# Performance work log

Measured on AMD Instinct MI355X. Metric: run time of the kernel, lower is better.

The kernel has to match this reference:

```python
import jax, jax.numpy as jnp
import numpy as np

B, NPG, D_IN, D, L = 64, 512, 1, 128, 10
N = B * NPG
DEG = 16
E = N * DEG
EPS = 1e-5


def setup_inputs() -> dict:
    key = jax.random.key(0)
    ks = jax.random.split(key, 8)
    x = jax.random.normal(ks[0], (N, D_IN), jnp.float32)
    # edges confined within each graph: local indices + per-graph offset
    src_local = jax.random.randint(ks[1], (E,), 0, NPG)
    dst_local = jax.random.randint(ks[2], (E,), 0, NPG)
    offs = (jnp.arange(E) // (E // B)) * NPG
    edge_src = (src_local + offs).astype(jnp.int32)
    edge_dst = (dst_local + offs).astype(jnp.int32)
    batch = jnp.repeat(jnp.arange(B, dtype=jnp.int32), NPG)
    g = lambda k, s, fan: jax.random.normal(k, s, jnp.float32) / np.float32(np.sqrt(fan))
    W0 = g(ks[3], (D_IN, D), D_IN)
    b0 = jnp.zeros((D,), jnp.float32)
    W_rest = g(ks[4], (L - 1, D, D), D)
    b_rest = jnp.zeros((L - 1, D), jnp.float32)
    gamma = jnp.ones((L, D), jnp.float32)
    beta = jnp.zeros((L, D), jnp.float32)
    W_att = g(ks[5], (D, D), D)
    return dict(x=x, edge_src=edge_src, edge_dst=edge_dst, batch=batch,
                W0=W0, b0=b0, W_rest=W_rest, b_rest=b_rest,
                gamma=gamma, beta=beta, W_att=W_att)


def _gcn_conv(h, W, b, src, dst, norm_e, self_w):
    # GCNConv: h' = D^-1/2 (A + I) D^-1/2 (h W) + b  (symmetric norm, self-loops)
    h = h @ W
    msg = norm_e[:, None] * h[src]                      # [E, D] gather
    agg = jax.ops.segment_sum(msg, dst, num_segments=N)  # [N, D] scatter-add
    return agg + self_w[:, None] * h + b


def _bn_relu(h, g, b):
    mu = jnp.mean(h, axis=0)
    var = jnp.var(h, axis=0)
    return jax.nn.relu(g * (h - mu) * jax.lax.rsqrt(var + EPS) + b)


def reference(x, edge_src, edge_dst, batch, W0, b0, W_rest, b_rest, gamma, beta, W_att):
    # symmetric GCN normalization with self-loops (edge weight 1)
    deg = 1.0 + jax.ops.segment_sum(jnp.ones((E,), x.dtype), edge_dst, num_segments=N)
    dinv = jax.lax.rsqrt(deg)
    norm_e = dinv[edge_src] * dinv[edge_dst]   # [E]
    self_w = dinv * dinv                        # [N] self-loop coefficient

    h = _gcn_conv(x, W0, b0, edge_src, edge_dst, norm_e, self_w)
    h = _bn_relu(h, gamma[0], beta[0])
    for l in range(L - 1):
        h = _gcn_conv(h, W_rest[l], b_rest[l], edge_src, edge_dst, norm_e, self_w)
        h = _bn_relu(h, gamma[l + 1], beta[l + 1])

    # graph attention pooling
    mean = jax.ops.segment_sum(h, batch, num_segments=B) / jnp.float32(NPG)  # [B, D]
    tg = jnp.tanh(mean @ W_att)                                              # [B, D]
    coefs = jax.nn.sigmoid(jnp.sum(h * tg[batch], axis=1) * 10.0)            # [N]
    graph_feat = jax.ops.segment_sum(coefs[:, None] * h, batch, num_segments=B)  # [B, D]

    # to_dense_batch (equal-sized graphs -> exact reshape) + concat broadcast graph feat
    node_dense = h.reshape(B, NPG, D)
    gf = jnp.broadcast_to(graph_feat[:, None, :], (B, NPG, D))
    return jnp.concatenate([node_dense, gf], axis=-1)  # [B, NPG, 2D]
```

## Files before the change

### kernel.cpp

```cpp
#include <hip/hip_runtime.h>
#include <hip/hip_bf16.h>
#include <math.h>

#define NN 32768
#define BG 64
#define NPGC 512
#define DD 128
#define EE 524288
#define LL 10
#define EPSF 1e-5f
#define PADK 72

typedef __attribute__((ext_vector_type(8))) short short8;
typedef __attribute__((ext_vector_type(4))) float float4v;

static __device__ __forceinline__ unsigned short f2bf(float x) {
    __hip_bfloat16 b = __float2bfloat16(x);
    return *reinterpret_cast<unsigned short*>(&b);
}
static __device__ __forceinline__ float bf2f(unsigned short u) {
    unsigned int v = ((unsigned int)u) << 16;
    return __uint_as_float(v);
}
static __device__ __forceinline__ void splitbf(float x, unsigned short& h, unsigned short& l) {
    unsigned short hh = f2bf(x);
    h = hh;
    l = f2bf(x - bf2f(hh));
}


__global__ void k_hist(const int* __restrict__ dst, int* __restrict__ cnt) {
    int e = blockIdx.x * 256 + threadIdx.x;
    atomicAdd(&cnt[dst[e]], 1);
}

__global__ void k_dinv(const int* __restrict__ cnt, float* __restrict__ dinv) {
    int n = blockIdx.x * 256 + threadIdx.x;
    dinv[n] = rsqrtf(1.0f + (float)cnt[n]);
}

__global__ void k_scan(const int* __restrict__ cnt, int* __restrict__ rp) {
    __shared__ int s[1024];
    int t = threadIdx.x;
    int loc[32];
    int base = t * 32, tot = 0;
    for (int i = 0; i < 32; i++) { loc[i] = cnt[base + i]; tot += loc[i]; }
    s[t] = tot;
    __syncthreads();
    for (int off = 1; off < 1024; off <<= 1) {
        int add = (t >= off) ? s[t - off] : 0;
        __syncthreads();
        s[t] += add;
        __syncthreads();
    }
    int ex = (t == 0) ? 0 : s[t - 1];
    for (int i = 0; i < 32; i++) { rp[base + i] = ex; ex += loc[i]; }
    if (t == 1023) rp[NN] = ex;
}

__global__ void k_fill(const int* __restrict__ src, const int* __restrict__ dst,
                       const float* __restrict__ dinv, const int* __restrict__ rp,
                       int* __restrict__ cursor, int* __restrict__ csr_src,
                       float* __restrict__ csr_w) {
    int e = blockIdx.x * 256 + threadIdx.x;
    int d = dst[e], sx = src[e];
    int p = atomicAdd(&cursor[d], 1);
    int i = rp[d] + p;
    csr_src[i] = sx;
    csr_w[i] = dinv[sx] * dinv[d];
}

__global__ __launch_bounds__(256) void k_adj(const int* __restrict__ rp,
        const int* __restrict__ csr_src, const float* __restrict__ csr_w,
        const float* __restrict__ dinv, unsigned short* __restrict__ Adj_h,
        unsigned short* __restrict__ Adj_l) {
    __shared__ float rowbuf[4][512];
    int t = threadIdx.x, lane = t & 63, wv = t >> 6;
    int n = blockIdx.x * 4 + wv;
    int nl = n & 511;
    for (int j = lane; j < 512; j += 64) rowbuf[wv][j] = 0.f;
    __syncthreads();
    int e1 = rp[n + 1];
    for (int e = rp[n] + lane; e < e1; e += 64)
        atomicAdd(&rowbuf[wv][csr_src[e] & 511], csr_w[e]);
    __syncthreads();
    if (lane == 0) rowbuf[wv][nl] += dinv[n] * dinv[n];
    __syncthreads();
    size_t base = (size_t)n * 512;
    for (int j = lane; j < 512; j += 64) {
        unsigned short h, l;
        splitbf(rowbuf[wv][j], h, l);
        Adj_h[base + j] = h;
        Adj_l[base + j] = l;
    }
}

__global__ void k_wt(const float* __restrict__ Wr, unsigned short* __restrict__ Wt_h,
                     unsigned short* __restrict__ Wt_l) {
    int idx = blockIdx.x * 256 + threadIdx.x;
    int l = idx >> 14, rem = idx & 16383;
    int fp = rem >> 7, f = rem & 127;
    unsigned short h, lo;
    splitbf(Wr[l * 16384 + f * 128 + fp], h, lo);
    Wt_h[idx] = h;
    Wt_l[idx] = lo;
}

__global__ void k_l0(const float* __restrict__ x, const float* __restrict__ W0,
                     unsigned short* __restrict__ hwT_h, unsigned short* __restrict__ hwT_l) {
    int u = blockIdx.x * 256 + threadIdx.x;
    int f = u >> 12, n0 = (u & 4095) * 8;
    float w = W0[f];
    float4 xa = *(const float4*)(x + n0);
    float4 xb = *(const float4*)(x + n0 + 4);
    float v[8] = {xa.x * w, xa.y * w, xa.z * w, xa.w * w,
                  xb.x * w, xb.y * w, xb.z * w, xb.w * w};
    unsigned short uh[8], ul[8];
    #pragma unroll
    for (int i = 0; i < 8; i++) splitbf(v[i], uh[i], ul[i]);
    *(uint4*)(hwT_h + (size_t)f * NN + n0) = *(uint4*)uh;
    *(uint4*)(hwT_l + (size_t)f * NN + n0) = *(uint4*)ul;
}

__global__ __launch_bounds__(256) void k_aggmm(const unsigned short* __restrict__ Adj_h,
        const unsigned short* __restrict__ Adj_l, const unsigned short* __restrict__ hwT_h,
        const unsigned short* __restrict__ hwT_l, const float* __restrict__ bias,
        float* __restrict__ pre, float* __restrict__ stats) {
    __shared__ unsigned short As_h[64 * PADK], As_l[64 * PADK];
    __shared__ unsigned short Bs_h[128 * PADK], Bs_l[128 * PADK];
    __shared__ float s_bias[128];
    __shared__ float s_sum[128], s_sq[128];
    int t = threadIdx.x, lane = t & 63, wv = t >> 6;
    int l15 = lane & 15, quad = lane >> 4;
    int b = blockIdx.x, r = b & 7, q = b >> 3;
    int g = r + 8 * (q & 7);
    int mb = (q >> 3) * 64;
    size_t arow = ((size_t)g * 512 + mb) * 512;
    size_t gcol = (size_t)g * 512;
    if (t < 128) { s_bias[t] = bias[t]; s_sum[t] = 0.f; s_sq[t] = 0.f; }
    float4v acc[8];
    #pragma unroll
    for (int i = 0; i < 8; i++) acc[i] = (float4v)0.f;

    for (int kc = 0; kc < 512; kc += 64) {
        __syncthreads();
        #pragma unroll
        for (int i = 0; i < 2; i++) {
            int u = t + i * 256;
            int row = u >> 3, ko = (u & 7) * 8;
            size_t go = arow + (size_t)row * 512 + kc + ko;
            *(uint4*)(&As_h[row * PADK + ko]) = *(const uint4*)(Adj_h + go);
            *(uint4*)(&As_l[row * PADK + ko]) = *(const uint4*)(Adj_l + go);
        }
        #pragma unroll
        for (int i = 0; i < 4; i++) {
            int u = t + i * 256;
            int f = u >> 3, ko = (u & 7) * 8;
            size_t go = (size_t)f * NN + gcol + kc + ko;
            *(uint4*)(&Bs_h[f * PADK + ko]) = *(const uint4*)(hwT_h + go);
            *(uint4*)(&Bs_l[f * PADK + ko]) = *(const uint4*)(hwT_l + go);
        }
        __syncthreads();
        int m0 = wv * 16;
        #pragma unroll
        for (int ks = 0; ks < 2; ks++) {
            int kb = ks * 32 + quad * 8;
            short8 ah = *(const short8*)(&As_h[(m0 + l15) * PADK + kb]);
            short8 al = *(const short8*)(&As_l[(m0 + l15) * PADK + kb]);
            #pragma unroll
            for (int nt = 0; nt < 8; nt++) {
                short8 bh = *(const short8*)(&Bs_h[(nt * 16 + l15) * PADK + kb]);
                short8 bl = *(const short8*)(&Bs_l[(nt * 16 + l15) * PADK + kb]);
                acc[nt] = __builtin_amdgcn_mfma_f32_16x16x32_bf16(ah, bh, acc[nt], 0, 0, 0);
                acc[nt] = __builtin_amdgcn_mfma_f32_16x16x32_bf16(ah, bl, acc[nt], 0, 0, 0);
                acc[nt] = __builtin_amdgcn_mfma_f32_16x16x32_bf16(al, bh, acc[nt], 0, 0, 0);
            }
        }
    }
    int n0 = g * 512 + mb + wv * 16 + quad * 4;
    #pragma unroll
    for (int nt = 0; nt < 8; nt++) {
        int f = nt * 16 + l15;
        float bf = s_bias[f];
        float cs = 0.f, cq = 0.f;
        #pragma unroll
        for (int rg = 0; rg < 4; rg++) {
            float v = acc[nt][rg] + bf;
            pre[(size_t)(n0 + rg) * 128 + f] = v;
            cs += v;
            cq = fmaf(v, v, cq);
        }
        cs += __shfl_xor(cs, 16); cs += __shfl_xor(cs, 32);
        cq += __shfl_xor(cq, 16); cq += __shfl_xor(cq, 32);
        if (quad == 0) { atomicAdd(&s_sum[f], cs); atomicAdd(&s_sq[f], cq); }
    }
    __syncthreads();
    if (t < 128) {
        atomicAdd(&stats[t], s_sum[t]);
        atomicAdd(&stats[128 + t], s_sq[t]);
    }
}

__global__ __launch_bounds__(256) void k_mmT(const float* __restrict__ pre,
        const float* __restrict__ stats, const float* __restrict__ gamma,
        const float* __restrict__ beta, const unsigned short* __restrict__ Wt_h,
        const unsigned short* __restrict__ Wt_l, unsigned short* __restrict__ hwT_h,
        unsigned short* __restrict__ hwT_l) {
    __shared__ unsigned short Ws_h[128 * PADK], Ws_l[128 * PADK];
    __shared__ unsigned short Xs_h[64 * PADK], Xs_l[64 * PADK];
    __shared__ float scL[256];
    int t = threadIdx.x, lane = t & 63, wv = t >> 6;
    int l15 = lane & 15, quad = lane >> 4;
    int b = blockIdx.x, r = b & 7, q = b >> 3;
    int g = r + 8 * (q & 7);
    int nb = g * NPGC + (q >> 3) * 64;
    if (t < 128) {
        float mu = stats[t] * (1.0f / NN);
        float var = stats[128 + t] * (1.0f / NN) - mu * mu;
        float s = gamma[t] * rsqrtf(var + EPSF);
        scL[t] = s;
        scL[128 + t] = fmaf(-mu, s, beta[t]);
    }
    float4v acc[8];
    #pragma unroll
    for (int i = 0; i < 8; i++) acc[i] = (float4v)0.f;

    for (int kc = 0; kc < 128; kc += 64) {
        __syncthreads();
        #pragma unroll
        for (int i = 0; i < 4; i++) {
            int u = t + i * 256;
            int fp = u >> 3, ko = (u & 7) * 8;
            int go = fp * 128 + kc + ko;
            *(uint4*)(&Ws_h[fp * PADK + ko]) = *(const uint4*)(Wt_h + go);
            *(uint4*)(&Ws_l[fp * PADK + ko]) = *(const uint4*)(Wt_l + go);
        }
        #pragma unroll
        for (int i = 0; i < 2; i++) {
            int u = t + i * 256;
            int n = u >> 3, fo = (u & 7) * 8;
            const float* pp = pre + (size_t)(nb + n) * 128 + kc + fo;
            float4 v0 = *(const float4*)(pp);
            float4 v1 = *(const float4*)(pp + 4);
            float4 s0 = *(const float4*)(&scL[kc + fo]);
            float4 s1 = *(const float4*)(&scL[kc + fo + 4]);
            float4 h0 = *(const float4*)(&scL[128 + kc + fo]);
            float4 h1 = *(const float4*)(&scL[128 + kc + fo + 4]);
            float v[8] = {fmaxf(fmaf(v0.x, s0.x, h0.x), 0.f),
                          fmaxf(fmaf(v0.y, s0.y, h0.y), 0.f),
                          fmaxf(fmaf(v0.z, s0.z, h0.z), 0.f),
                          fmaxf(fmaf(v0.w, s0.w, h0.w), 0.f),
                          fmaxf(fmaf(v1.x, s1.x, h1.x), 0.f),
                          fmaxf(fmaf(v1.y, s1.y, h1.y), 0.f),
                          fmaxf(fmaf(v1.z, s1.z, h1.z), 0.f),
                          fmaxf(fmaf(v1.w, s1.w, h1.w), 0.f)};
            unsigned short uh[8], ul[8];
            #pragma unroll
            for (int j = 0; j < 8; j++) splitbf(v[j], uh[j], ul[j]);
            *(uint4*)(&Xs_h[n * PADK + fo]) = *(uint4*)uh;
            *(uint4*)(&Xs_l[n * PADK + fo]) = *(uint4*)ul;
        }
        __syncthreads();
        int m0 = wv * 32;
        #pragma unroll
        for (int ks = 0; ks < 2; ks++) {
            int kb = ks * 32 + quad * 8;
            short8 a0h = *(const short8*)(&Ws_h[(m0 + l15) * PADK + kb]);
            short8 a0l = *(const short8*)(&Ws_l[(m0 + l15) * PADK + kb]);
            short8 a1h = *(const short8*)(&Ws_h[(m0 + 16 + l15) * PADK + kb]);
            short8 a1l = *(const short8*)(&Ws_l[(m0 + 16 + l15) * PADK + kb]);
            #pragma unroll
            for (int nt = 0; nt < 4; nt++) {
                short8 bh = *(const short8*)(&Xs_h[(nt * 16 + l15) * PADK + kb]);
                short8 bl = *(const short8*)(&Xs_l[(nt * 16 + l15) * PADK + kb]);
                acc[nt]     = __builtin_amdgcn_mfma_f32_16x16x32_bf16(a0h, bh, acc[nt], 0, 0, 0);
                acc[nt]     = __builtin_amdgcn_mfma_f32_16x16x32_bf16(a0h, bl, acc[nt], 0, 0, 0);
                acc[nt]     = __builtin_amdgcn_mfma_f32_16x16x32_bf16(a0l, bh, acc[nt], 0, 0, 0);
                acc[4 + nt] = __builtin_amdgcn_mfma_f32_16x16x32_bf16(a1h, bh, acc[4 + nt], 0, 0, 0);
                acc[4 + nt] = __builtin_amdgcn_mfma_f32_16x16x32_bf16(a1h, bl, acc[4 + nt], 0, 0, 0);
                acc[4 + nt] = __builtin_amdgcn_mfma_f32_16x16x32_bf16(a1l, bh, acc[4 + nt], 0, 0, 0);
            }
        }
    }
    #pragma unroll
    for (int mt = 0; mt < 2; mt++) {
        #pragma unroll
        for (int nt = 0; nt < 4; nt++) {
            int n = nb + nt * 16 + l15;
            int fp0 = wv * 32 + mt * 16 + quad * 4;
            float4v a = acc[mt * 4 + nt];
            #pragma unroll
            for (int rg = 0; rg < 4; rg++) {
                unsigned short h, lo;
                splitbf(a[rg], h, lo);
                hwT_h[(size_t)(fp0 + rg) * NN + n] = h;
                hwT_l[(size_t)(fp0 + rg) * NN + n] = lo;
            }
        }
    }
}

__global__ __launch_bounds__(256) void k_bn_pool(float* __restrict__ pre,
        const float* __restrict__ stats, const float* __restrict__ gamma,
        const float* __restrict__ beta, float* __restrict__ meansum) {
    __shared__ float ssum[256];
    __shared__ float scL[256];
    int t = threadIdx.x;
    int b = blockIdx.x, r = b & 7, q = b >> 3;
    int g = r + 8 * (q & 7);
    int nb = g * NPGC + (q >> 3) * 64;
    if (t < 128) {
        float mu = stats[t] * (1.0f / NN);
        float var = stats[128 + t] * (1.0f / NN) - mu * mu;
        float s = gamma[t] * rsqrtf(var + EPSF);
        scL[t] = s;
        scL[128 + t] = fmaf(-mu, s, beta[t]);
    }
    __syncthreads();
    int f = t & 127;
    float s = scL[f], sh = scL[128 + f];
    float lsum = 0.f;
    int base = nb * 128;
    for (int i = 0; i < 32; i++) {
        int idx = base + i * 256 + t;
        float v = fmaxf(fmaf(pre[idx], s, sh), 0.f);
        pre[idx] = v;
        lsum += v;
    }
    ssum[t] = lsum;
    __syncthreads();
    if (t < 128) atomicAdd(&meansum[g * 128 + f], ssum[t] + ssum[t + 128]);
}

__global__ void k_tg(const float* __restrict__ meansum, const float* __restrict__ Watt,
                     float* __restrict__ tg) {
    __shared__ float m[128];
    int g = blockIdx.x, t = threadIdx.x;
    m[t] = meansum[g * 128 + t] * (1.0f / NPGC);
    __syncthreads();
    float a2 = 0.f;
    for (int k = 0; k < 128; k++) a2 = fmaf(m[k], Watt[k * 128 + t], a2);
    tg[g * 128 + t] = tanhf(a2);
}

__global__ __launch_bounds__(256) void k_coef_gf(const float* __restrict__ h,
        const float* __restrict__ tg, float* __restrict__ gf) {
    __shared__ float tgs[128];
    __shared__ float coef[64];
    int t = threadIdx.x;
    int b = blockIdx.x, r = b & 7, q = b >> 3;
    int g = r + 8 * (q & 7);
    int n0 = (q >> 3) * 64;
    if (t < 128) tgs[t] = tg[g * 128 + t];
    __syncthreads();
    int wid = t >> 6, lane = t & 63;
    const float* hp = h + (size_t)g * NPGC * 128;
    for (int j = wid; j < 64; j += 4) {
        int n = n0 + j;
        float p = hp[n * 128 + lane] * tgs[lane] + hp[n * 128 + 64 + lane] * tgs[64 + lane];
        for (int off = 32; off; off >>= 1) p += __shfl_xor(p, off);
        if (lane == 0) coef[j] = 1.0f / (1.0f + expf(-10.0f * p));
    }
    __syncthreads();
    int f = t & 127, half = t >> 7;
    float acc = 0.f;
    for (int j = 0; j < 32; j++) {
        int jj = half * 32 + j;
        acc = fmaf(coef[jj], hp[(n0 + jj) * 128 + f], acc);
    }
    atomicAdd(&gf[g * 128 + f], acc);
}

__global__ void k_out(const float* __restrict__ h, const float* __restrict__ gf,
                      float* __restrict__ out) {
    int idx = blockIdx.x * 256 + threadIdx.x;
    int c4 = (idx & 63) * 4;
    int n = idx >> 6;
    int g = n >> 9;
    float4 v = (c4 < 128) ? *(const float4*)(h + (size_t)n * 128 + c4)
                          : *(const float4*)(gf + g * 128 + (c4 - 128));
    *(float4*)(out + (size_t)idx * 4) = v;
}

extern "C" void kernel_launch(void* const* d_in, const int* in_sizes, int n_in,
                              void* d_out, int out_size, void* d_ws, size_t ws_size,
                              hipStream_t stream) {
    const float* x     = (const float*)d_in[0];
    const int*   esrc  = (const int*)d_in[1];
    const int*   edst  = (const int*)d_in[2];
    const float* W0    = (const float*)d_in[4];
    const float* b0    = (const float*)d_in[5];
    const float* Wr    = (const float*)d_in[6];
    const float* br    = (const float*)d_in[7];
    const float* gamma = (const float*)d_in[8];
    const float* beta  = (const float*)d_in[9];
    const float* Watt  = (const float*)d_in[10];
    float* out = (float*)d_out;
    float* ws  = (float*)d_ws;

    int*   cnt     = (int*)(ws + 0);
    int*   cursor  = (int*)(ws + 32768);
    int*   rp      = (int*)(ws + 65536);
    float* dinv    = ws + 98560;
    float* stats   = ws + 131584;
    float* tgbuf   = ws + 134400;
    float* meansum = ws + 142592;
    float* gf      = ws + 150784;
    unsigned short* Wt_h  = (unsigned short*)(ws + 159232);
    unsigned short* Wt_l  = (unsigned short*)(ws + 232960);
    unsigned short* hwT_h = (unsigned short*)(ws + 306688);
    unsigned short* hwT_l = (unsigned short*)(ws + 2403840);
    unsigned short* Adj_h = (unsigned short*)(ws + 4500992);
    unsigned short* Adj_l = (unsigned short*)(ws + 12889600);
    float* pre     = ws + 21278208;
    int*   csr_src = (int*)pre;
    float* csr_w   = pre + EE;

    hipMemsetAsync(cnt, 0, NN * sizeof(int), stream);
    hipMemsetAsync(cursor, 0, NN * sizeof(int), stream);
    hipMemsetAsync(stats, 0, LL * 256 * sizeof(float), stream);
    hipMemsetAsync(meansum, 0, BG * 128 * sizeof(float), stream);
    hipMemsetAsync(gf, 0, BG * 128 * sizeof(float), stream);

    k_hist<<<EE / 256, 256, 0, stream>>>(edst, cnt);
    k_dinv<<<NN / 256, 256, 0, stream>>>(cnt, dinv);
    k_scan<<<1, 1024, 0, stream>>>(cnt, rp);
    k_fill<<<EE / 256, 256, 0, stream>>>(esrc, edst, dinv, rp, cursor, csr_src, csr_w);
    k_adj<<<NN / 4, 256, 0, stream>>>(rp, csr_src, csr_w, dinv, Adj_h, Adj_l);
    k_wt<<<9 * 16384 / 256, 256, 0, stream>>>(Wr, Wt_h, Wt_l);
    k_l0<<<128 * (NN / 8) / 256, 256, 0, stream>>>(x, W0, hwT_h, hwT_l);

    for (int l = 0; l < LL; l++) {
        const float* bias = (l == 0) ? b0 : br + (l - 1) * DD;
        k_aggmm<<<NN / 64, 256, 0, stream>>>(Adj_h, Adj_l, hwT_h, hwT_l, bias,
                                             pre, stats + l * 256);
        if (l < LL - 1)
            k_mmT<<<NN / 64, 256, 0, stream>>>(pre, stats + l * 256, gamma + l * DD,
                                               beta + l * DD, Wt_h + l * 16384,
                                               Wt_l + l * 16384, hwT_h, hwT_l);
        else
            k_bn_pool<<<NN / 64, 256, 0, stream>>>(pre, stats + l * 256, gamma + l * DD,
                                                   beta + l * DD, meansum);
    }
    k_tg<<<BG, 128, 0, stream>>>(meansum, Watt, tgbuf);
    k_coef_gf<<<NN / 64, 256, 0, stream>>>(pre, tgbuf, gf);
    k_out<<<NN * 64 / 256, 256, 0, stream>>>(pre, gf, out);
}
```

Before: 595.5 us.

## Factor degree normalization out of adjacency to use exact integer-count bf16 matrix

Replaces the normalized float adjacency, which was stored as a hi/lo bf16 pair, with a plain edge-count matrix plus identity. Counts are small integers and are exact in a single bf16, so the low half and its MFMAs are dropped. The dinv scaling is applied on both sides instead: in the hwT producers (k_l0, k_mmT) and in the aggregation epilogue. CSR construction (scan, fill, adj kernels) is replaced by a direct atomic histogram into a dense int matrix, which costs a 64MB memset and a conversion pass. The MFMA work is also reorganized per wave, and block-level stats reduction now uses global atomics directly.

```diff
diff --git a/kernel.cpp b/kernel.cpp
--- a/kernel.cpp
+++ b/kernel.cpp
@@ -29,9 +29,12 @@
 }
 
 
-__global__ void k_hist(const int* __restrict__ dst, int* __restrict__ cnt) {
+__global__ void k_histM(const int* __restrict__ src, const int* __restrict__ dst,
+                        int* __restrict__ Mint, int* __restrict__ cnt) {
     int e = blockIdx.x * 256 + threadIdx.x;
-    atomicAdd(&cnt[dst[e]], 1);
+    int d = dst[e], s = src[e] & 511;
+    atomicAdd(&Mint[(size_t)d * 512 + s], 1);
+    atomicAdd(&cnt[d], 1);
 }
 
 __global__ void k_dinv(const int* __restrict__ cnt, float* __restrict__ dinv) {
@@ -39,60 +42,18 @@
     dinv[n] = rsqrtf(1.0f + (float)cnt[n]);
 }
 
-__global__ void k_scan(const int* __restrict__ cnt, int* __restrict__ rp) {
-    __shared__ int s[1024];
-    int t = threadIdx.x;
-    int loc[32];
-    int base = t * 32, tot = 0;
-    for (int i = 0; i < 32; i++) { loc[i] = cnt[base + i]; tot += loc[i]; }
-    s[t] = tot;
-    __syncthreads();
-    for (int off = 1; off < 1024; off <<= 1) {
-        int add = (t >= off) ? s[t - off] : 0;
-        __syncthreads();
-        s[t] += add;
-        __syncthreads();
-    }
-    int ex = (t == 0) ? 0 : s[t - 1];
-    for (int i = 0; i < 32; i++) { rp[base + i] = ex; ex += loc[i]; }
-    if (t == 1023) rp[NN] = ex;
-}
-
-__global__ void k_fill(const int* __restrict__ src, const int* __restrict__ dst,
-                       const float* __restrict__ dinv, const int* __restrict__ rp,
-                       int* __restrict__ cursor, int* __restrict__ csr_src,
-                       float* __restrict__ csr_w) {
-    int e = blockIdx.x * 256 + threadIdx.x;
-    int d = dst[e], sx = src[e];
-    int p = atomicAdd(&cursor[d], 1);
-    int i = rp[d] + p;
-    csr_src[i] = sx;
-    csr_w[i] = dinv[sx] * dinv[d];
-}
-
-__global__ __launch_bounds__(256) void k_adj(const int* __restrict__ rp,
-        const int* __restrict__ csr_src, const float* __restrict__ csr_w,
-        const float* __restrict__ dinv, unsigned short* __restrict__ Adj_h,
-        unsigned short* __restrict__ Adj_l) {
-    __shared__ float rowbuf[4][512];
-    int t = threadIdx.x, lane = t & 63, wv = t >> 6;
-    int n = blockIdx.x * 4 + wv;
-    int nl = n & 511;
-    for (int j = lane; j < 512; j += 64) rowbuf[wv][j] = 0.f;
-    __syncthreads();
-    int e1 = rp[n + 1];
-    for (int e = rp[n] + lane; e < e1; e += 64)
-        atomicAdd(&rowbuf[wv][csr_src[e] & 511], csr_w[e]);
-    __syncthreads();
-    if (lane == 0) rowbuf[wv][nl] += dinv[n] * dinv[n];
-    __syncthreads();
-    size_t base = (size_t)n * 512;
-    for (int j = lane; j < 512; j += 64) {
-        unsigned short h, l;
-        splitbf(rowbuf[wv][j], h, l);
-        Adj_h[base + j] = h;
-        Adj_l[base + j] = l;
-    }
+__global__ void k_conv(const int* __restrict__ Mint, unsigned short* __restrict__ Mh) {
+    int idx = (blockIdx.x * 256 + threadIdx.x) * 4;
+    int4 v = *(const int4*)(Mint + idx);
+    int row = idx >> 9;
+    int diag = row & 511;
+    int cb = idx & 511;
+    unsigned short us[4];
+    us[0] = f2bf((float)(v.x + (cb + 0 == diag ? 1 : 0)));
+    us[1] = f2bf((float)(v.y + (cb + 1 == diag ? 1 : 0)));
+    us[2] = f2bf((float)(v.z + (cb + 2 == diag ? 1 : 0)));
+    us[3] = f2bf((float)(v.w + (cb + 3 == diag ? 1 : 0)));
+    *(uint2*)(Mh + idx) = *(uint2*)us;
 }
 
 __global__ void k_wt(const float* __restrict__ Wr, unsigned short* __restrict__ Wt_h,
@@ -107,14 +68,17 @@
 }
 
 __global__ void k_l0(const float* __restrict__ x, const float* __restrict__ W0,
+                     const float* __restrict__ dinv,
                      unsigned short* __restrict__ hwT_h, unsigned short* __restrict__ hwT_l) {
     int u = blockIdx.x * 256 + threadIdx.x;
     int f = u >> 12, n0 = (u & 4095) * 8;
     float w = W0[f];
     float4 xa = *(const float4*)(x + n0);
     float4 xb = *(const float4*)(x + n0 + 4);
-    float v[8] = {xa.x * w, xa.y * w, xa.z * w, xa.w * w,
-                  xb.x * w, xb.y * w, xb.z * w, xb.w * w};
+    float4 da = *(const float4*)(dinv + n0);
+    float4 db = *(const float4*)(dinv + n0 + 4);
+    float v[8] = {xa.x * w * da.x, xa.y * w * da.y, xa.z * w * da.z, xa.w * w * da.w,
+                  xb.x * w * db.x, xb.y * w * db.y, xb.z * w * db.z, xb.w * w * db.w};
     unsigned short uh[8], ul[8];
     #pragma unroll
     for (int i = 0; i < 8; i++) splitbf(v[i], uh[i], ul[i]);
@@ -122,14 +86,12 @@
     *(uint4*)(hwT_l + (size_t)f * NN + n0) = *(uint4*)ul;
 }
 
-__global__ __launch_bounds__(256) void k_aggmm(const unsigned short* __restrict__ Adj_h,
-        const unsigned short* __restrict__ Adj_l, const unsigned short* __restrict__ hwT_h,
-        const unsigned short* __restrict__ hwT_l, const float* __restrict__ bias,
+__global__ __launch_bounds__(256) void k_aggmm(const unsigned short* __restrict__ Mh,
+        const unsigned short* __restrict__ hwT_h, const unsigned short* __restrict__ hwT_l,
+        const float* __restrict__ dinv, const float* __restrict__ bias,
         float* __restrict__ pre, float* __restrict__ stats) {
-    __shared__ unsigned short As_h[64 * PADK], As_l[64 * PADK];
+    __shared__ unsigned short As[64 * PADK];
     __shared__ unsigned short Bs_h[128 * PADK], Bs_l[128 * PADK];
-    __shared__ float s_bias[128];
-    __shared__ float s_sum[128], s_sq[128];
     int t = threadIdx.x, lane = t & 63, wv = t >> 6;
     int l15 = lane & 15, quad = lane >> 4;
     int b = blockIdx.x, r = b & 7, q = b >> 3;
@@ -137,7 +99,6 @@
     int mb = (q >> 3) * 64;
     size_t arow = ((size_t)g * 512 + mb) * 512;
     size_t gcol = (size_t)g * 512;
-    if (t < 128) { s_bias[t] = bias[t]; s_sum[t] = 0.f; s_sq[t] = 0.f; }
     float4v acc[8];
     #pragma unroll
     for (int i = 0; i < 8; i++) acc[i] = (float4v)0.f;
@@ -148,9 +109,8 @@
         for (int i = 0; i < 2; i++) {
             int u = t + i * 256;
             int row = u >> 3, ko = (u & 7) * 8;
-            size_t go = arow + (size_t)row * 512 + kc + ko;
-            *(uint4*)(&As_h[row * PADK + ko]) = *(const uint4*)(Adj_h + go);
-            *(uint4*)(&As_l[row * PADK + ko]) = *(const uint4*)(Adj_l + go);
+            *(uint4*)(&As[row * PADK + ko]) =
+                *(const uint4*)(Mh + arow + (size_t)row * 512 + kc + ko);
         }
         #pragma unroll
         for (int i = 0; i < 4; i++) {
@@ -161,51 +121,66 @@
             *(uint4*)(&Bs_l[f * PADK + ko]) = *(const uint4*)(hwT_l + go);
         }
         __syncthreads();
-        int m0 = wv * 16;
+        int f0 = wv * 32;
         #pragma unroll
         for (int ks = 0; ks < 2; ks++) {
             int kb = ks * 32 + quad * 8;
-            short8 ah = *(const short8*)(&As_h[(m0 + l15) * PADK + kb]);
-            short8 al = *(const short8*)(&As_l[(m0 + l15) * PADK + kb]);
+            short8 a0 = *(const short8*)(&As[(l15) * PADK + kb]);
+            short8 a1 = *(const short8*)(&As[(16 + l15) * PADK + kb]);
+            short8 a2 = *(const short8*)(&As[(32 + l15) * PADK + kb]);
+            short8 a3 = *(const short8*)(&As[(48 + l15) * PADK + kb]);
             #pragma unroll
-            for (int nt = 0; nt < 8; nt++) {
-                short8 bh = *(const short8*)(&Bs_h[(nt * 16 + l15) * PADK + kb]);
-                short8 bl = *(const short8*)(&Bs_l[(nt * 16 + l15) * PADK + kb]);
-                acc[nt] = __builtin_amdgcn_mfma_f32_16x16x32_bf16(ah, bh, acc[nt], 0, 0, 0);
-                acc[nt] = __builtin_amdgcn_mfma_f32_16x16x32_bf16(ah, bl, acc[nt], 0, 0, 0);
-                acc[nt] = __builtin_amdgcn_mfma_f32_16x16x32_bf16(al, bh, acc[nt], 0, 0, 0);
+            for (int nt = 0; nt < 2; nt++) {
+                short8 bh = *(const short8*)(&Bs_h[(f0 + nt * 16 + l15) * PADK + kb]);
+                short8 bl = *(const short8*)(&Bs_l[(f0 + nt * 16 + l15) * PADK + kb]);
+                acc[0 + nt] = __builtin_amdgcn_mfma_f32_16x16x32_bf16(a0, bh, acc[0 + nt], 0, 0, 0);
+                acc[0 + nt] = __builtin_amdgcn_mfma_f32_16x16x32_bf16(a0, bl, acc[0 + nt], 0, 0, 0);
+                acc[2 + nt] = __builtin_amdgcn_mfma_f32_16x16x32_bf16(a1, bh, acc[2 + nt], 0, 0, 0);
+                acc[2 + nt] = __builtin_amdgcn_mfma_f32_16x16x32_bf16(a1, bl, acc[2 + nt], 0, 0, 0);
+                acc[4 + nt] = __builtin_amdgcn_mfma_f32_16x16x32_bf16(a2, bh, acc[4 + nt], 0, 0, 0);
+                acc[4 + nt] = __builtin_amdgcn_mfma_f32_16x16x32_bf16(a2, bl, acc[4 + nt], 0, 0, 0);
+                acc[6 + nt] = __builtin_amdgcn_mfma_f32_16x16x32_bf16(a3, bh, acc[6 + nt], 0, 0, 0);
+                acc[6 + nt] = __builtin_amdgcn_mfma_f32_16x16x32_bf16(a3, bl, acc[6 + nt], 0, 0, 0);
             }
         }
     }
-    int n0 = g * 512 + mb + wv * 16 + quad * 4;
+    int gbase = g * 512 + mb;
     #pragma unroll
-    for (int nt = 0; nt < 8; nt++) {
-        int f = nt * 16 + l15;
-        float bf = s_bias[f];
+    for (int nt = 0; nt < 2; nt++) {
+        int f = wv * 32 + nt * 16 + l15;
+        float bf = bias[f];
         float cs = 0.f, cq = 0.f;
         #pragma unroll
-        for (int rg = 0; rg < 4; rg++) {
-            float v = acc[nt][rg] + bf;
-            pre[(size_t)(n0 + rg) * 128 + f] = v;
-            cs += v;
-            cq = fmaf(v, v, cq);
+        for (int mt = 0; mt < 4; mt++) {
+            int n0 = gbase + mt * 16 + quad * 4;
+            float4 dv = *(const float4*)(dinv + n0);
+            float4v a = acc[mt * 2 + nt];
+            float v0 = fmaf(dv.x, a[0], bf);
+            float v1 = fmaf(dv.y, a[1], bf);
+            float v2 = fmaf(dv.z, a[2], bf);
+            float v3 = fmaf(dv.w, a[3], bf);
+            pre[(size_t)(n0 + 0) * 128 + f] = v0;
+            pre[(size_t)(n0 + 1) * 128 + f] = v1;
+            pre[(size_t)(n0 + 2) * 128 + f] = v2;
+            pre[(size_t)(n0 + 3) * 128 + f] = v3;
+            cs += v0 + v1 + v2 + v3;
+            cq = fmaf(v0, v0, cq); cq = fmaf(v1, v1, cq);
+            cq = fmaf(v2, v2, cq); cq = fmaf(v3, v3, cq);
         }
         cs += __shfl_xor(cs, 16); cs += __shfl_xor(cs, 32);
         cq += __shfl_xor(cq, 16); cq += __shfl_xor(cq, 32);
-        if (quad == 0) { atomicAdd(&s_sum[f], cs); atomicAdd(&s_sq[f], cq); }
-    }
-    __syncthreads();
-    if (t < 128) {
-        atomicAdd(&stats[t], s_sum[t]);
-        atomicAdd(&stats[128 + t], s_sq[t]);
+        if (quad == 0) {
+            atomicAdd(&stats[f], cs);
+            atomicAdd(&stats[128 + f], cq);
+        }
     }
 }
 
 __global__ __launch_bounds__(256) void k_mmT(const float* __restrict__ pre,
         const float* __restrict__ stats, const float* __restrict__ gamma,
-        const float* __restrict__ beta, const unsigned short* __restrict__ Wt_h,
-        const unsigned short* __restrict__ Wt_l, unsigned short* __restrict__ hwT_h,
-        unsigned short* __restrict__ hwT_l) {
+        const float* __restrict__ beta, const float* __restrict__ dinv,
+        const unsigned short* __restrict__ Wt_h, const unsigned short* __restrict__ Wt_l,
+        unsigned short* __restrict__ hwT_h, unsigned short* __restrict__ hwT_l) {
     __shared__ unsigned short Ws_h[128 * PADK], Ws_l[128 * PADK];
     __shared__ unsigned short Xs_h[64 * PADK], Xs_l[64 * PADK];
     __shared__ float scL[256];
@@ -287,12 +262,13 @@
         #pragma unroll
         for (int nt = 0; nt < 4; nt++) {
             int n = nb + nt * 16 + l15;
+            float dv = dinv[n];
             int fp0 = wv * 32 + mt * 16 + quad * 4;
             float4v a = acc[mt * 4 + nt];
             #pragma unroll
             for (int rg = 0; rg < 4; rg++) {
                 unsigned short h, lo;
-                splitbf(a[rg], h, lo);
+                splitbf(dv * a[rg], h, lo);
                 hwT_h[(size_t)(fp0 + rg) * NN + n] = h;
                 hwT_l[(size_t)(fp0 + rg) * NN + n] = lo;
             }
@@ -399,44 +375,38 @@
     float* ws  = (float*)d_ws;
 
     int*   cnt     = (int*)(ws + 0);
-    int*   cursor  = (int*)(ws + 32768);
-    int*   rp      = (int*)(ws + 65536);
-    float* dinv    = ws + 98560;
-    float* stats   = ws + 131584;
-    float* tgbuf   = ws + 134400;
-    float* meansum = ws + 142592;
-    float* gf      = ws + 150784;
-    unsigned short* Wt_h  = (unsigned short*)(ws + 159232);
-    unsigned short* Wt_l  = (unsigned short*)(ws + 232960);
-    unsigned short* hwT_h = (unsigned short*)(ws + 306688);
-    unsigned short* hwT_l = (unsigned short*)(ws + 2403840);
-    unsigned short* Adj_h = (unsigned short*)(ws + 4500992);
-    unsigned short* Adj_l = (unsigned short*)(ws + 12889600);
-    float* pre     = ws + 21278208;
-    int*   csr_src = (int*)pre;
-    float* csr_w   = pre + EE;
+    float* dinv    = ws + 32768;
+    float* stats   = ws + 65536;
+    float* tgbuf   = ws + 68096;
+    float* meansum = ws + 76288;
+    float* gf      = ws + 84480;
+    unsigned short* Wt_h  = (unsigned short*)(ws + 92672);
+    unsigned short* Wt_l  = (unsigned short*)(ws + 166400);
+    unsigned short* hwT_h = (unsigned short*)(ws + 240128);
+    unsigned short* hwT_l = (unsigned short*)(ws + 2337280);
+    unsigned short* Mh    = (unsigned short*)(ws + 4434432);
+    int*   Mint    = (int*)(ws + 12823040);
+    float* pre     = ws + 12823040;
 
     hipMemsetAsync(cnt, 0, NN * sizeof(int), stream);
-    hipMemsetAsync(cursor, 0, NN * sizeof(int), stream);
     hipMemsetAsync(stats, 0, LL * 256 * sizeof(float), stream);
     hipMemsetAsync(meansum, 0, BG * 128 * sizeof(float), stream);
     hipMemsetAsync(gf, 0, BG * 128 * sizeof(float), stream);
-
-    k_hist<<<EE / 256, 256, 0, stream>>>(edst, cnt);
+    hipMemsetAsync(Mint, 0, (size_t)NN * 512 * sizeof(int), stream);
+
+    k_histM<<<EE / 256, 256, 0, stream>>>(esrc, edst, Mint, cnt);
     k_dinv<<<NN / 256, 256, 0, stream>>>(cnt, dinv);
-    k_scan<<<1, 1024, 0, stream>>>(cnt, rp);
-    k_fill<<<EE / 256, 256, 0, stream>>>(esrc, edst, dinv, rp, cursor, csr_src, csr_w);
-    k_adj<<<NN / 4, 256, 0, stream>>>(rp, csr_src, csr_w, dinv, Adj_h, Adj_l);
+    k_conv<<<NN * 512 / 1024, 256, 0, stream>>>(Mint, Mh);
     k_wt<<<9 * 16384 / 256, 256, 0, stream>>>(Wr, Wt_h, Wt_l);
-    k_l0<<<128 * (NN / 8) / 256, 256, 0, stream>>>(x, W0, hwT_h, hwT_l);
+    k_l0<<<128 * (NN / 8) / 256, 256, 0, stream>>>(x, W0, dinv, hwT_h, hwT_l);
 
     for (int l = 0; l < LL; l++) {
         const float* bias = (l == 0) ? b0 : br + (l - 1) * DD;
-        k_aggmm<<<NN / 64, 256, 0, stream>>>(Adj_h, Adj_l, hwT_h, hwT_l, bias,
+        k_aggmm<<<NN / 64, 256, 0, stream>>>(Mh, hwT_h, hwT_l, dinv, bias,
                                              pre, stats + l * 256);
         if (l < LL - 1)
             k_mmT<<<NN / 64, 256, 0, stream>>>(pre, stats + l * 256, gamma + l * DD,
-                                               beta + l * DD, Wt_h + l * 16384,
+                                               beta + l * DD, dinv, Wt_h + l * 16384,
                                                Wt_l + l * 16384, hwT_h, hwT_l);
         else
             k_bn_pool<<<NN / 64, 256, 0, stream>>>(pre, stats + l * 256, gamma + l * DD,
```

Result: faster. 538.9 us (-9.5%).
